# Kernel tuning notes

Hardware: AMD Instinct MI355X
Metric: run time of the kernel (lower is better)

## Reference

```python
import jax, jax.numpy as jnp
import numpy as np

B, CIN, CE, CA, N, S = 2, 64, 128, 128, 1024, 32
SCALE = np.sqrt(np.float32(CA))  # scale_mode == 'dimfts'


def _vnlin(W, x):
    # VNLinear: linear map over the channel dim of (B, C, 3, N, S)
    return jnp.einsum('oc,bcdns->bodns', W, x)


def setup_inputs() -> dict:
    key = jax.random.key(0)
    ks = jax.random.split(key, 16)
    def w(k, o, i):
        return (jax.random.normal(k, (o, i), jnp.float32) / np.sqrt(np.float32(i)))
    return {
        'group_xyz': jax.random.normal(ks[0], (B, N, S, 3), jnp.float32),
        'group_fts': jax.random.normal(ks[1], (B, CIN, 3, N, S), jnp.float32),
        'query_xyz': jax.random.normal(ks[2], (B, N, 3), jnp.float32),
        'W_e1': w(ks[3], CE, CIN), 'W_e2': w(ks[4], CE, CE),
        'W_q': w(ks[5], CA, CE), 'W_k': w(ks[6], CA, CE), 'W_v': w(ks[7], CA, CE),
        'W_r1': w(ks[8], 64, 1), 'W_r2': w(ks[9], CA, 64),
        'W_std': w(ks[10], 3, CA),
        'W_f1': w(ks[11], CA, CA * 3), 'b_f1': jax.random.normal(ks[12], (CA,), jnp.float32) * 0.02,
        'W_f2': w(ks[13], CA, CA), 'b_f2': jax.random.normal(ks[14], (CA,), jnp.float32) * 0.02,
    }


def reference(group_xyz, group_fts, query_xyz, W_e1, W_e2, W_q, W_k, W_v,
              W_r1, W_r2, W_std, W_f1, b_f1, W_f2, b_f2):
    # vnn_e: two stacked VNLinear layers
    group_emb = _vnlin(W_e2, _vnlin(W_e1, group_fts))        # (B, CE, 3, N, S)
    query_emb = group_emb[..., :1]                           # (B, CE, 3, N, 1)
    q = _vnlin(W_q, query_emb)                               # (B, CA, 3, N, 1)
    k = _vnlin(W_k, group_emb)                               # (B, CA, 3, N, S)
    v = _vnlin(W_v, group_emb)                               # (B, CA, 3, N, S)

    # positional relation: xyz_rel -> (B, 1, 3, N, S) -> vnn_r
    xyz_rel = group_xyz - query_xyz[:, :, None, :]           # (B, N, S, 3)
    xyz_rel = jnp.transpose(xyz_rel[:, :, :, None, :], (0, 3, 4, 1, 2))  # (B,1,3,N,S)
    pos_rel = _vnlin(W_r2, _vnlin(W_r1, xyz_rel))            # (B, CA, 3, N, S)

    # relation_func == 'sub'
    attn = q - k + pos_rel                                   # (B, CA, 3, N, S)

    # VNStdFeatureLin (dim=5, no frame normalization): z0 = VNLinear(CA->3)
    z0 = _vnlin(W_std, attn)                                 # (B, 3, 3, N, S)
    attn = jnp.einsum('bijns,bjkns->bikns', attn, z0)        # (B, CA, 3, N, S) invariant

    # attn_fwd: 1x1 conv -> ReLU -> 1x1 conv on (B, CA*3, N, S)
    attn = attn.reshape(B, CA * 3, N, S)
    h = jax.nn.relu(jnp.einsum('oc,bcns->bons', W_f1, attn) + b_f1[:, None, None])
    a = jnp.einsum('oc,bcns->bons', W_f2, h) + b_f2[:, None, None]  # (B, CA, N, S)

    a = jax.nn.softmax(a[:, :, None, :, :] / SCALE, axis=-1)  # (B, CA, 1, N, S)
    v = v + pos_rel
    resi = jnp.sum(a * v, axis=-1)                            # (B, CA, 3, N)
    return resi
```

## Files before the change

### kernel.cpp

```cpp
#include <hip/hip_runtime.h>
#include <hip/hip_bf16.h>
#include <math.h>

typedef __hip_bfloat16  bf16;
typedef __hip_bfloat162 bf162;
typedef __attribute__((ext_vector_type(8))) short short8;
typedef __attribute__((ext_vector_type(4))) float f32x4;

#define BB   2
#define CINC 64
#define NN   1024
#define SSS  32
#define NS   (NN * SSS)

#define OFF_WE21 0
#define OFF_WR   8192
#define OFF_KBA  8320
#define OFF_VB   16512
#define OFF_F1B  20608
#define OFF_F2B  45184
#define WS_NEED_FLOATS 53376

#define S_ATT_B  0
#define S_FTS_B  26112
#define S_XYZ_B  39936
#define SMEM_BYTES 40128

__device__ __forceinline__ float bf2f(short s) {
    unsigned int u = ((unsigned int)(unsigned short)s) << 16;
    return __uint_as_float(u);
}
__device__ __forceinline__ short f2bf(float f) {
    bf16 h = __float2bfloat16(f);
    return *reinterpret_cast<short*>(&h);
}
__device__ __forceinline__ unsigned pk2(float a, float b) {
    bf162 p = __float22bfloat162_rn(make_float2(a, b));
    return *reinterpret_cast<unsigned*>(&p);
}

__global__ __launch_bounds__(256) void prep1(const float* __restrict__ We1,
                                             const float* __restrict__ We2,
                                             float* __restrict__ ws) {
    int e = blockIdx.x * 256 + threadIdx.x;
    int o = e >> 6, c = e & 63;
    float acc = 0.f;
    for (int m = 0; m < 128; ++m)
        acc = fmaf(We2[o * 128 + m], We1[m * 64 + c], acc);
    ws[OFF_WE21 + o * 64 + c] = acc;
}

__global__ __launch_bounds__(256) void prep2(const float* __restrict__ Wq,
                                             const float* __restrict__ Wk,
                                             const float* __restrict__ Wv,
                                             const float* __restrict__ Wr1,
                                             const float* __restrict__ Wr2,
                                             const float* __restrict__ Wf1,
                                             const float* __restrict__ Wf2,
                                             float* __restrict__ ws) {
    const float* we21 = ws + OFF_WE21;
    int e = blockIdx.x * 256 + threadIdx.x;
    if (e < 16384) {
        int i = e >> 7, c2 = e & 127;
        const float* W = (c2 < 64) ? Wk : Wq;
        int c = c2 & 63;
        float acc = 0.f;
        for (int o = 0; o < 128; ++o)
            acc = fmaf(W[i * 128 + o], we21[o * 64 + c], acc);
        if (c2 >= 64) acc = -acc;
        ((bf16*)(ws + OFF_KBA))[i * 128 + c2] = __float2bfloat16(acc);
    } else if (e < 24576) {
        int le = e - 16384;
        int i = le >> 6, c = le & 63;
        float acc = 0.f;
        for (int o = 0; o < 128; ++o)
            acc = fmaf(Wv[i * 128 + o], we21[o * 64 + c], acc);
        ((bf16*)(ws + OFF_VB))[i * 64 + c] = __float2bfloat16(acc);
    } else if (e < 24704) {
        int i = e - 24576;
        float acc = 0.f;
        for (int m = 0; m < 64; ++m)
            acc = fmaf(Wr2[i * 64 + m], Wr1[m], acc);
        ws[OFF_WR + i] = acc;
    } else if (e < 24704 + 49152) {
        int f = e - 24704;
        int o = f / 384, kp = f - o * 384;
        int c = (kp & 127) * 3 + (kp >> 7);
        ((bf16*)(ws + OFF_F1B))[f] = __float2bfloat16(Wf1[o * 384 + c]);
    } else if (e < 24704 + 49152 + 16384) {
        int f = e - (24704 + 49152);
        ((bf16*)(ws + OFF_F2B))[f] = __float2bfloat16(Wf2[f]);
    }
}

__global__ __launch_bounds__(256, 4) void fused_main(
        const float* __restrict__ gxyz, const float* __restrict__ gfts,
        const float* __restrict__ qxyz, const float* __restrict__ Wstd,
        const float* __restrict__ bf1,  const float* __restrict__ bf2,
        const float* __restrict__ ws,   float* __restrict__ out) {
    extern __shared__ char smc[];
    short* s_att  = (short*)(smc + S_ATT_B);
    short* h_t    = s_att;
    short* a_t    = s_att + 4352;
    short* fts_s  = (short*)(smc + S_FTS_B);
    short* s_xyzh = (short*)(smc + S_XYZ_B);
    float* s_red  = (float*)(smc + S_ATT_B);

    const int t    = threadIdx.x;
    const int bid  = blockIdx.x;
    const int b    = bid >> 10;
    const int n    = bid & 1023;
    const int w    = t >> 6;
    const int lane = t & 63;
    const int quad = lane >> 4;
    const int lq   = lane & 15;
    const int wb   = 32 * w;

    const float* gb = gfts + (size_t)b * (CINC * 3 * NS) + n * SSS;
    const short* kba = (const short*)(ws + OFF_KBA);

    const int cp = t >> 3;
    const int ml = (t & 7) * 4;

    short8 Ka[2][2];
    #pragma unroll
    for (int it = 0; it < 2; ++it) {
        int i = wb + it * 16 + lq;
        #pragma unroll
        for (int kc = 0; kc < 2; ++kc)
            Ka[it][kc] = *(const short8*)(kba + i * 128 + kc * 32 + quad * 8);
    }
    float4 wr2v[2] = { *(const float4*)(ws + OFF_WR + wb + quad * 4),
                       *(const float4*)(ws + OFF_WR + wb + 16 + quad * 4) };
    float wr2[2] = { ws[OFF_WR + wb + lq], ws[OFF_WR + wb + 16 + lq] };

    {
        const float* fb = gb + (2 * cp * 3 + 0) * NS + ml;
        float4 f0 = *(const float4*)(fb);
        float4 f1 = *(const float4*)(fb + 3 * NS);
        short* dst = fts_s + (0 * 32 + ml) * 72 + 2 * cp;
        *(unsigned*)(dst)       = pk2(f0.x, f1.x);
        *(unsigned*)(dst + 72)  = pk2(f0.y, f1.y);
        *(unsigned*)(dst + 144) = pk2(f0.z, f1.z);
        *(unsigned*)(dst + 216) = pk2(f0.w, f1.w);
        if (t >= 160) {
            int id = t - 160;
            int d = id >> 5, s = id & 31;
            s_xyzh[id] = f2bf(gxyz[((b * NN + n) * SSS + s) * 3 + d]
                              - qxyz[(b * NN + n) * 3 + d]);
        }
    }
    __syncthreads();

    #pragma unroll
    for (int h = 0; h < 3; ++h) {
        float4 g0, g1;
        if (h < 2) {
            const float* fb = gb + (2 * cp * 3 + h + 1) * NS + ml;
            g0 = *(const float4*)(fb);
            g1 = *(const float4*)(fb + 3 * NS);
        }

        f32x4 qa[2];
        {
            const short* qp = fts_s + (h * 32) * 72 + quad * 8;
            short8 aq0 = *(const short8*)(qp);
            short8 aq1 = *(const short8*)(qp + 32);
            #pragma unroll
            for (int it = 0; it < 2; ++it) {
                int i = wb + it * 16 + lq;
                short8 kq2 = *(const short8*)(kba + i * 128 + 64 + quad * 8);
                short8 kq3 = *(const short8*)(kba + i * 128 + 96 + quad * 8);
                f32x4 z = {0.f, 0.f, 0.f, 0.f};
                z = __builtin_amdgcn_mfma_f32_16x16x32_bf16(kq2, aq0, z, 0, 0, 0);
                z = __builtin_amdgcn_mfma_f32_16x16x32_bf16(kq3, aq1, z, 0, 0, 0);
                qa[it] = z;
            }
        }
        #pragma unroll
        for (int mt_h = 0; mt_h < 2; ++mt_h) {
            int m = h * 32 + mt_h * 16 + lq;
            const short* ap = fts_s + m * 72 + quad * 8;
            short8 a0 = *(const short8*)(ap);
            short8 a1 = *(const short8*)(ap + 32);
            float xm = bf2f(s_xyzh[m]);
            #pragma unroll
            for (int it = 0; it < 2; ++it) {
                f32x4 kk = {0.f, 0.f, 0.f, 0.f};
                kk = __builtin_amdgcn_mfma_f32_16x16x32_bf16(Ka[it][0], a0, kk, 0, 0, 0);
                kk = __builtin_amdgcn_mfma_f32_16x16x32_bf16(Ka[it][1], a1, kk, 0, 0, 0);
                float p[4];
                #pragma unroll
                for (int reg = 0; reg < 4; ++reg)
                    p[reg] = wr2v[it][reg] * xm - kk[reg] - qa[it][reg];
                uint2 pk;
                pk.x = pk2(p[0], p[1]);
                pk.y = pk2(p[2], p[3]);
                *(uint2*)(s_att + m * 136 + wb + it * 16 + quad * 4) = pk;
            }
        }

        if (h < 2) {
            short* dst = fts_s + ((h + 1) * 32 + ml) * 72 + 2 * cp;
            *(unsigned*)(dst)       = pk2(g0.x, g1.x);
            *(unsigned*)(dst + 72)  = pk2(g0.y, g1.y);
            *(unsigned*)(dst + 144) = pk2(g0.z, g1.z);
            *(unsigned*)(dst + 216) = pk2(g0.w, g1.w);
        }
        __syncthreads();
    }

    {
        short8 As[4];
        #pragma unroll
        for (int kc = 0; kc < 4; ++kc) {
            short8 a = {0, 0, 0, 0, 0, 0, 0, 0};
            if (lq < 3) {
                const float* wp = Wstd + lq * 128 + kc * 32 + quad * 8;
                float4 w0 = *(const float4*)(wp);
                float4 w1 = *(const float4*)(wp + 4);
                a[0] = f2bf(w0.x); a[1] = f2bf(w0.y); a[2] = f2bf(w0.z); a[3] = f2bf(w0.w);
                a[4] = f2bf(w1.x); a[5] = f2bf(w1.y); a[6] = f2bf(w1.z); a[7] = f2bf(w1.w);
            }
            As[kc] = a;
        }
        for (int tile = w; tile < 6; tile += 4) {
            f32x4 acc = {0.f, 0.f, 0.f, 0.f};
            const short* bp = s_att + (tile * 16 + lq) * 136 + quad * 8;
            #pragma unroll
            for (int kc = 0; kc < 4; ++kc) {
                short8 bfr = *(const short8*)(bp + kc * 32);
                acc = __builtin_amdgcn_mfma_f32_16x16x32_bf16(As[kc], bfr, acc, 0, 0, 0);
            }
            if (quad == 0) {
                float* hp = (float*)(fts_s + (tile * 16 + lq) * 72 + 64);
                #pragma unroll
                for (int reg = 0; reg < 3; ++reg)
                    hp[reg] = acc[reg];
            }
        }
    }
    __syncthreads();

    for (int u = t; u < 512; u += 256) {
        int s  = u >> 4;
        int i0 = (u & 15) * 8;
        float z[3][3];
        #pragma unroll
        for (int kk = 0; kk < 3; ++kk) {
            const float* hp = (const float*)(fts_s + (kk * 32 + s) * 72 + 64);
            #pragma unroll
            for (int j = 0; j < 3; ++j)
                z[j][kk] = hp[j];
        }
        float af[3][8];
        #pragma unroll
        for (int j = 0; j < 3; ++j) {
            short8 v8 = *(const short8*)(s_att + (j * 32 + s) * 136 + i0);
            #pragma unroll
            for (int x = 0; x < 8; ++x) af[j][x] = bf2f(v8[x]);
        }
        #pragma unroll
        for (int kk = 0; kk < 3; ++kk) {
            short8 o8;
            #pragma unroll
            for (int x = 0; x < 8; ++x)
                o8[x] = f2bf(af[0][x] * z[0][kk] + af[1][x] * z[1][kk] + af[2][x] * z[2][kk]);
            *(short8*)(s_att + (kk * 32 + s) * 136 + i0) = o8;
        }
    }
    __syncthreads();

    f32x4 eacc[2][2];
    {
        f32x4 zz = {0.f, 0.f, 0.f, 0.f};
        eacc[0][0] = zz; eacc[0][1] = zz; eacc[1][0] = zz; eacc[1][1] = zz;
        const short* f1b = (const short*)(ws + OFF_F1B);
        const short* ab0 = f1b + (wb + lq) * 384 + quad * 8;
        const short* ab1 = ab0 + 16 * 384;
        #pragma unroll 2
        for (int ks = 0; ks < 12; ++ks) {
            int kk = ks >> 2;
            int ic = (ks & 3) * 32 + quad * 8;
            short8 a0 = *(const short8*)(ab0 + ks * 32);
            short8 a1 = *(const short8*)(ab1 + ks * 32);
            const short* bp = s_att + (kk * 32) * 136 + ic;
            short8 b0 = *(const short8*)(bp + lq * 136);
            short8 b1 = *(const short8*)(bp + (lq + 16) * 136);
            eacc[0][0] = __builtin_amdgcn_mfma_f32_16x16x32_bf16(a0, b0, eacc[0][0], 0, 0, 0);
            eacc[0][1] = __builtin_amdgcn_mfma_f32_16x16x32_bf16(a0, b1, eacc[0][1], 0, 0, 0);
            eacc[1][0] = __builtin_amdgcn_mfma_f32_16x16x32_bf16(a1, b0, eacc[1][0], 0, 0, 0);
            eacc[1][1] = __builtin_amdgcn_mfma_f32_16x16x32_bf16(a1, b1, eacc[1][1], 0, 0, 0);
        }
    }
    __syncthreads();

    #pragma unroll
    for (int mt = 0; mt < 2; ++mt) {
        int ob = wb + mt * 16 + quad * 4;
        float4 bb = *(const float4*)(bf1 + ob);
        float bv[4] = {bb.x, bb.y, bb.z, bb.w};
        #pragma unroll
        for (int nt = 0; nt < 2; ++nt) {
            f32x4 c = eacc[mt][nt];
            int s = nt * 16 + lq;
            uint2 pk;
            pk.x = pk2(fmaxf(c[0] + bv[0], 0.f), fmaxf(c[1] + bv[1], 0.f));
            pk.y = pk2(fmaxf(c[2] + bv[2], 0.f), fmaxf(c[3] + bv[3], 0.f));
            *(uint2*)(h_t + s * 136 + ob) = pk;
        }
    }
    __syncthreads();

    {
        f32x4 facc[2][2];
        f32x4 zz = {0.f, 0.f, 0.f, 0.f};
        facc[0][0] = zz; facc[0][1] = zz; facc[1][0] = zz; facc[1][1] = zz;
        const short* f2b = (const short*)(ws + OFF_F2B);
        const short* ab0 = f2b + (wb + lq) * 128 + quad * 8;
        const short* ab1 = ab0 + 16 * 128;
        #pragma unroll 2
        for (int ks = 0; ks < 4; ++ks) {
            int c0 = ks * 32 + quad * 8;
            short8 a0 = *(const short8*)(ab0 + ks * 32);
            short8 a1 = *(const short8*)(ab1 + ks * 32);
            short8 b0 = *(const short8*)(h_t + lq * 136 + c0);
            short8 b1 = *(const short8*)(h_t + (lq + 16) * 136 + c0);
            facc[0][0] = __builtin_amdgcn_mfma_f32_16x16x32_bf16(a0, b0, facc[0][0], 0, 0, 0);
            facc[0][1] = __builtin_amdgcn_mfma_f32_16x16x32_bf16(a0, b1, facc[0][1], 0, 0, 0);
            facc[1][0] = __builtin_amdgcn_mfma_f32_16x16x32_bf16(a1, b0, facc[1][0], 0, 0, 0);
            facc[1][1] = __builtin_amdgcn_mfma_f32_16x16x32_bf16(a1, b1, facc[1][1], 0, 0, 0);
        }
        const float inv = 0.08838834764831845f;
        #pragma unroll
        for (int mt = 0; mt < 2; ++mt) {
            int ob = wb + mt * 16 + quad * 4;
            float4 bb = *(const float4*)(bf2 + ob);
            float bv[4] = {bb.x, bb.y, bb.z, bb.w};
            float a0v[4], a1v[4];
            #pragma unroll
            for (int reg = 0; reg < 4; ++reg) {
                float v0 = facc[mt][0][reg] + bv[reg];
                float v1 = facc[mt][1][reg] + bv[reg];
                float mx = fmaxf(v0, v1);
                mx = fmaxf(mx, __shfl_xor(mx, 1));
                mx = fmaxf(mx, __shfl_xor(mx, 2));
                mx = fmaxf(mx, __shfl_xor(mx, 4));
                mx = fmaxf(mx, __shfl_xor(mx, 8));
                float e0 = __expf((v0 - mx) * inv);
                float e1 = __expf((v1 - mx) * inv);
                float sm = e0 + e1;
                sm += __shfl_xor(sm, 1);
                sm += __shfl_xor(sm, 2);
                sm += __shfl_xor(sm, 4);
                sm += __shfl_xor(sm, 8);
                float rs = 1.f / sm;
                a0v[reg] = e0 * rs;
                a1v[reg] = e1 * rs;
            }
            uint2 pk;
            pk.x = pk2(a0v[0], a0v[1]);
            pk.y = pk2(a0v[2], a0v[3]);
            *(uint2*)(a_t + lq * 136 + ob) = pk;
            pk.x = pk2(a1v[0], a1v[1]);
            pk.y = pk2(a1v[2], a1v[3]);
            *(uint2*)(a_t + (16 + lq) * 136 + ob) = pk;
        }
    }
    __syncthreads();

    {
        __builtin_amdgcn_sched_barrier(0);
        short8 Va[2][2];
        {
            const short* vbb = (const short*)(ws + OFF_VB);
            #pragma unroll
            for (int it = 0; it < 2; ++it) {
                int i = wb + it * 16 + lq;
                #pragma unroll
                for (int kc = 0; kc < 2; ++kc)
                    Va[it][kc] = *(const short8*)(vbb + i * 64 + kc * 32 + quad * 8);
            }
        }
        float pr[2][3];
        #pragma unroll
        for (int it = 0; it < 2; ++it)
            #pragma unroll
            for (int d = 0; d < 3; ++d) pr[it][d] = 0.f;
        #pragma unroll
        for (int mt = 0; mt < 6; ++mt) {
            int d  = mt >> 1;
            int s0 = (mt & 1) * 16 + quad * 4;
            const short* ap = fts_s + (mt * 16 + lq) * 72 + quad * 8;
            short8 a0 = *(const short8*)(ap);
            short8 a1 = *(const short8*)(ap + 32);
            #pragma unroll
            for (int it = 0; it < 2; ++it) {
                f32x4 vv = {0.f, 0.f, 0.f, 0.f};
                vv = __builtin_amdgcn_mfma_f32_16x16x32_bf16(a0, Va[it][0], vv, 0, 0, 0);
                vv = __builtin_amdgcn_mfma_f32_16x16x32_bf16(a1, Va[it][1], vv, 0, 0, 0);
                int i = wb + it * 16 + lq;
                #pragma unroll
                for (int reg = 0; reg < 4; ++reg) {
                    int m = mt * 16 + quad * 4 + reg;
                    float vp = vv[reg] + wr2[it] * bf2f(s_xyzh[m]);
                    pr[it][d] = fmaf(bf2f(a_t[(s0 + reg) * 136 + i]), vp, pr[it][d]);
                }
            }
        }
        #pragma unroll
        for (int it = 0; it < 2; ++it)
            #pragma unroll
            for (int d = 0; d < 3; ++d) {
                float v = pr[it][d];
                v += __shfl_xor(v, 16);
                v += __shfl_xor(v, 32);
                if (quad == 0) s_red[(wb + it * 16 + lq) * 3 + d] = v;
            }
    }
    __syncthreads();

    for (int e = t; e < 384; e += 256)
        out[(b * 384 + e) * NN + n] = s_red[e];
}

extern "C" void kernel_launch(void* const* d_in, const int* in_sizes, int n_in,
                              void* d_out, int out_size, void* d_ws, size_t ws_size,
                              hipStream_t stream) {
    const float* gxyz = (const float*)d_in[0];
    const float* gfts = (const float*)d_in[1];
    const float* qxyz = (const float*)d_in[2];
    const float* We1  = (const float*)d_in[3];
    const float* We2  = (const float*)d_in[4];
    const float* Wq   = (const float*)d_in[5];
    const float* Wk   = (const float*)d_in[6];
    const float* Wv   = (const float*)d_in[7];
    const float* Wr1  = (const float*)d_in[8];
    const float* Wr2  = (const float*)d_in[9];
    const float* Wstd = (const float*)d_in[10];
    const float* bf1  = (const float*)d_in[12];
    const float* bf2  = (const float*)d_in[14];
    float* out = (float*)d_out;
    float* ws  = (float*)d_ws;

    (void)hipFuncSetAttribute((const void*)fused_main,
                              hipFuncAttributeMaxDynamicSharedMemorySize, SMEM_BYTES);

    prep1<<<32, 256, 0, stream>>>(We1, We2, ws);
    prep2<<<353, 256, 0, stream>>>(Wq, Wk, Wv, Wr1, Wr2,
                                   (const float*)d_in[11], (const float*)d_in[13], ws);
    fused_main<<<BB * NN, 256, SMEM_BYTES, stream>>>(gxyz, gfts, qxyz, Wstd,
                                                     bf1, bf2, ws, out);
}
```

Measured before the change: 179.2 us.

## Fold VNStd projection into precomputed weights and transpose softmax scratch layout

A new prep kernel precomputes W_std composed with the key/query weights and the positional vector, so z0 is produced directly from input features by two spare waves inside the h loop. This removes the separate z0 MFMA stage and one block-wide barrier. The softmax output is also stored transposed so the final reduction reads four weights in one vector load instead of strided scalars. Block indices are remapped to interleave blocks, and the packed bf16 stores are restructured. The extra waves add MFMA work inside the h loop, and the fold introduces bf16 rounding of the combined weights.

```diff
diff --git a/kernel.cpp b/kernel.cpp
--- a/kernel.cpp
+++ b/kernel.cpp
@@ -93,6 +93,27 @@
     }
 }
 
+__global__ __launch_bounds__(256) void prep3(const float* __restrict__ Wstd,
+                                             float* __restrict__ ws) {
+    int e = blockIdx.x * 256 + threadIdx.x;
+    if (e < 2048) {
+        int j = e >> 7, c2 = e & 127;
+        float acc = 0.f;
+        if (j < 3) {
+            const short* kba = (const short*)(ws + OFF_KBA);
+            for (int i = 0; i < 128; ++i)
+                acc = fmaf(Wstd[j * 128 + i], bf2f(kba[i * 128 + c2]), acc);
+        }
+        ((bf16*)(ws + OFF_WE21))[e] = __float2bfloat16(acc);
+    } else if (e < 2051) {
+        int j = e - 2048;
+        float acc = 0.f;
+        for (int i = 0; i < 128; ++i)
+            acc = fmaf(Wstd[j * 128 + i], ws[OFF_WR + i], acc);
+        ws[OFF_WE21 + 1024 + j] = acc;
+    }
+}
+
 __global__ __launch_bounds__(256, 4) void fused_main(
         const float* __restrict__ gxyz, const float* __restrict__ gfts,
         const float* __restrict__ qxyz, const float* __restrict__ Wstd,
@@ -101,13 +122,14 @@
     extern __shared__ char smc[];
     short* s_att  = (short*)(smc + S_ATT_B);
     short* h_t    = s_att;
-    short* a_t    = s_att + 4352;
+    short* a_tt   = s_att + 4352;
     short* fts_s  = (short*)(smc + S_FTS_B);
     short* s_xyzh = (short*)(smc + S_XYZ_B);
     float* s_red  = (float*)(smc + S_ATT_B);
 
     const int t    = threadIdx.x;
-    const int bid  = blockIdx.x;
+    const int bid0 = blockIdx.x;
+    const int bid  = ((bid0 & 7) << 8) | (bid0 >> 3);
     const int b    = bid >> 10;
     const int n    = bid & 1023;
     const int w    = t >> 6;
@@ -118,6 +140,7 @@
 
     const float* gb = gfts + (size_t)b * (CINC * 3 * NS) + n * SSS;
     const short* kba = (const short*)(ws + OFF_KBA);
+    const short* wka = (const short*)(ws + OFF_WE21);
 
     const int cp = t >> 3;
     const int ml = (t & 7) * 4;
@@ -133,6 +156,16 @@
     float4 wr2v[2] = { *(const float4*)(ws + OFF_WR + wb + quad * 4),
                        *(const float4*)(ws + OFF_WR + wb + 16 + quad * 4) };
     float wr2[2] = { ws[OFF_WR + wb + lq], ws[OFF_WR + wb + 16 + lq] };
+    short8 WA[4];
+    float wwr[3];
+    if (w >= 2) {
+        #pragma unroll
+        for (int kc = 0; kc < 4; ++kc)
+            WA[kc] = *(const short8*)(wka + lq * 128 + kc * 32 + quad * 8);
+        wwr[0] = ws[OFF_WE21 + 1024];
+        wwr[1] = ws[OFF_WE21 + 1025];
+        wwr[2] = ws[OFF_WE21 + 1026];
+    }
 
     {
         const float* fb = gb + (2 * cp * 3 + 0) * NS + ml;
@@ -161,21 +194,20 @@
             g1 = *(const float4*)(fb + 3 * NS);
         }
 
+        const short* qp = fts_s + (h * 32) * 72 + quad * 8;
+        short8 aq0 = *(const short8*)(qp);
+        short8 aq1 = *(const short8*)(qp + 32);
+
         f32x4 qa[2];
-        {
-            const short* qp = fts_s + (h * 32) * 72 + quad * 8;
-            short8 aq0 = *(const short8*)(qp);
-            short8 aq1 = *(const short8*)(qp + 32);
-            #pragma unroll
-            for (int it = 0; it < 2; ++it) {
-                int i = wb + it * 16 + lq;
-                short8 kq2 = *(const short8*)(kba + i * 128 + 64 + quad * 8);
-                short8 kq3 = *(const short8*)(kba + i * 128 + 96 + quad * 8);
-                f32x4 z = {0.f, 0.f, 0.f, 0.f};
-                z = __builtin_amdgcn_mfma_f32_16x16x32_bf16(kq2, aq0, z, 0, 0, 0);
-                z = __builtin_amdgcn_mfma_f32_16x16x32_bf16(kq3, aq1, z, 0, 0, 0);
-                qa[it] = z;
-            }
+        #pragma unroll
+        for (int it = 0; it < 2; ++it) {
+            int i = wb + it * 16 + lq;
+            short8 kq2 = *(const short8*)(kba + i * 128 + 64 + quad * 8);
+            short8 kq3 = *(const short8*)(kba + i * 128 + 96 + quad * 8);
+            f32x4 z = {0.f, 0.f, 0.f, 0.f};
+            z = __builtin_amdgcn_mfma_f32_16x16x32_bf16(kq2, aq0, z, 0, 0, 0);
+            z = __builtin_amdgcn_mfma_f32_16x16x32_bf16(kq3, aq1, z, 0, 0, 0);
+            qa[it] = z;
         }
         #pragma unroll
         for (int mt_h = 0; mt_h < 2; ++mt_h) {
@@ -198,6 +230,19 @@
                 pk.y = pk2(p[2], p[3]);
                 *(uint2*)(s_att + m * 136 + wb + it * 16 + quad * 4) = pk;
             }
+            if (w == 2 + mt_h) {
+                f32x4 z2 = {0.f, 0.f, 0.f, 0.f};
+                z2 = __builtin_amdgcn_mfma_f32_16x16x32_bf16(WA[0], a0,  z2, 0, 0, 0);
+                z2 = __builtin_amdgcn_mfma_f32_16x16x32_bf16(WA[1], a1,  z2, 0, 0, 0);
+                z2 = __builtin_amdgcn_mfma_f32_16x16x32_bf16(WA[2], aq0, z2, 0, 0, 0);
+                z2 = __builtin_amdgcn_mfma_f32_16x16x32_bf16(WA[3], aq1, z2, 0, 0, 0);
+                if (quad == 0) {
+                    float* hp = (float*)(fts_s + m * 72 + 64);
+                    #pragma unroll
+                    for (int reg = 0; reg < 3; ++reg)
+                        hp[reg] = xm * wwr[reg] - z2[reg];
+                }
+            }
         }
 
         if (h < 2) {
@@ -210,38 +255,6 @@
         __syncthreads();
     }
 
-    {
-        short8 As[4];
-        #pragma unroll
-        for (int kc = 0; kc < 4; ++kc) {
-            short8 a = {0, 0, 0, 0, 0, 0, 0, 0};
-            if (lq < 3) {
-                const float* wp = Wstd + lq * 128 + kc * 32 + quad * 8;
-                float4 w0 = *(const float4*)(wp);
-                float4 w1 = *(const float4*)(wp + 4);
-                a[0] = f2bf(w0.x); a[1] = f2bf(w0.y); a[2] = f2bf(w0.z); a[3] = f2bf(w0.w);
-                a[4] = f2bf(w1.x); a[5] = f2bf(w1.y); a[6] = f2bf(w1.z); a[7] = f2bf(w1.w);
-            }
-            As[kc] = a;
-        }
-        for (int tile = w; tile < 6; tile += 4) {
-            f32x4 acc = {0.f, 0.f, 0.f, 0.f};
-            const short* bp = s_att + (tile * 16 + lq) * 136 + quad * 8;
-            #pragma unroll
-            for (int kc = 0; kc < 4; ++kc) {
-                short8 bfr = *(const short8*)(bp + kc * 32);
-                acc = __builtin_amdgcn_mfma_f32_16x16x32_bf16(As[kc], bfr, acc, 0, 0, 0);
-            }
-            if (quad == 0) {
-                float* hp = (float*)(fts_s + (tile * 16 + lq) * 72 + 64);
-                #pragma unroll
-                for (int reg = 0; reg < 3; ++reg)
-                    hp[reg] = acc[reg];
-            }
-        }
-    }
-    __syncthreads();
-
     for (int u = t; u < 512; u += 256) {
         int s  = u >> 4;
         int i0 = (u & 15) * 8;
@@ -262,11 +275,21 @@
         }
         #pragma unroll
         for (int kk = 0; kk < 3; ++kk) {
-            short8 o8;
-            #pragma unroll
-            for (int x = 0; x < 8; ++x)
-                o8[x] = f2bf(af[0][x] * z[0][kk] + af[1][x] * z[1][kk] + af[2][x] * z[2][kk]);
-            *(short8*)(s_att + (kk * 32 + s) * 136 + i0) = o8;
+            float q0, q1;
+            uint4 o4;
+            q0 = af[0][0] * z[0][kk] + af[1][0] * z[1][kk] + af[2][0] * z[2][kk];
+            q1 = af[0][1] * z[0][kk] + af[1][1] * z[1][kk] + af[2][1] * z[2][kk];
+            o4.x = pk2(q0, q1);
+            q0 = af[0][2] * z[0][kk] + af[1][2] * z[1][kk] + af[2][2] * z[2][kk];
+            q1 = af[0][3] * z[0][kk] + af[1][3] * z[1][kk] + af[2][3] * z[2][kk];
+            o4.y = pk2(q0, q1);
+            q0 = af[0][4] * z[0][kk] + af[1][4] * z[1][kk] + af[2][4] * z[2][kk];
+            q1 = af[0][5] * z[0][kk] + af[1][5] * z[1][kk] + af[2][5] * z[2][kk];
+            o4.z = pk2(q0, q1);
+            q0 = af[0][6] * z[0][kk] + af[1][6] * z[1][kk] + af[2][6] * z[2][kk];
+            q1 = af[0][7] * z[0][kk] + af[1][7] * z[1][kk] + af[2][7] * z[2][kk];
+            o4.w = pk2(q0, q1);
+            *(uint4*)(s_att + (kk * 32 + s) * 136 + i0) = o4;
         }
     }
     __syncthreads();
@@ -358,13 +381,15 @@
                 a0v[reg] = e0 * rs;
                 a1v[reg] = e1 * rs;
             }
-            uint2 pk;
-            pk.x = pk2(a0v[0], a0v[1]);
-            pk.y = pk2(a0v[2], a0v[3]);
-            *(uint2*)(a_t + lq * 136 + ob) = pk;
-            pk.x = pk2(a1v[0], a1v[1]);
-            pk.y = pk2(a1v[2], a1v[3]);
-            *(uint2*)(a_t + (16 + lq) * 136 + ob) = pk;
+            #pragma unroll
+            for (int pr = 0; pr < 2; ++pr) {
+                unsigned u0 = pk2(a0v[2 * pr], a0v[2 * pr + 1]);
+                unsigned u1 = pk2(a1v[2 * pr], a1v[2 * pr + 1]);
+                a_tt[(ob + 2 * pr)     * 40 + lq]      = (short)(u0 & 0xffff);
+                a_tt[(ob + 2 * pr + 1) * 40 + lq]      = (short)(u0 >> 16);
+                a_tt[(ob + 2 * pr)     * 40 + 16 + lq] = (short)(u1 & 0xffff);
+                a_tt[(ob + 2 * pr + 1) * 40 + 16 + lq] = (short)(u1 >> 16);
+            }
         }
     }
     __syncthreads();
@@ -400,11 +425,14 @@
                 vv = __builtin_amdgcn_mfma_f32_16x16x32_bf16(a0, Va[it][0], vv, 0, 0, 0);
                 vv = __builtin_amdgcn_mfma_f32_16x16x32_bf16(a1, Va[it][1], vv, 0, 0, 0);
                 int i = wb + it * 16 + lq;
+                uint2 av = *(const uint2*)(a_tt + i * 40 + s0);
+                float aw[4] = { bf2f((short)(av.x & 0xffff)), bf2f((short)(av.x >> 16)),
+                                bf2f((short)(av.y & 0xffff)), bf2f((short)(av.y >> 16)) };
                 #pragma unroll
                 for (int reg = 0; reg < 4; ++reg) {
                     int m = mt * 16 + quad * 4 + reg;
                     float vp = vv[reg] + wr2[it] * bf2f(s_xyzh[m]);
-                    pr[it][d] = fmaf(bf2f(a_t[(s0 + reg) * 136 + i]), vp, pr[it][d]);
+                    pr[it][d] = fmaf(aw[reg], vp, pr[it][d]);
                 }
             }
         }
@@ -449,6 +477,7 @@
     prep1<<<32, 256, 0, stream>>>(We1, We2, ws);
     prep2<<<353, 256, 0, stream>>>(Wq, Wk, Wv, Wr1, Wr2,
                                    (const float*)d_in[11], (const float*)d_in[13], ws);
+    prep3<<<9, 256, 0, stream>>>(Wstd, ws);
     fused_main<<<BB * NN, 256, SMEM_BYTES, stream>>>(gxyz, gfts, qxyz, Wstd,
                                                      bf1, bf2, ws, out);
 }
```

Result: no change. 177.4 us (-1.0%).
